# Kernel tuning notes

Hardware: AMD Instinct MI355X
Metric: run time of the kernel (lower is better)

## Reference

```python
import jax, jax.numpy as jnp
import numpy as np

B, C, T = 8, 256, 8192
K, DIL = 2, 2            # kernel_size, dilation (layer_i=1)
CAUSE = (K - 1) * DIL    # shift_diff when pad_input == 0


def _dconv(x, w, b):
    # dilated causal-style Conv1d, VALID padding: (B,C,T) -> (B,C,T-CAUSE)
    y = jax.lax.conv_general_dilated(
        x, w, window_strides=(1,), padding='VALID',
        rhs_dilation=(DIL,), dimension_numbers=('NCH', 'OIH', 'NCH'))
    return y + b[None, :, None]


def setup_inputs() -> dict:
    key = jax.random.key(0)
    ks = jax.random.split(key, 20)
    f = lambda k, s: jax.random.normal(k, s, dtype=jnp.float32)
    w = lambda k, s: f(k, s) * 0.05
    return {
        'x': f(ks[0], (B, C, T)),
        'cin': f(ks[1], (B, C, T)),
        'gin': f(ks[2], (B, C, T)),
        'skips': f(ks[3], (B, C, T)),
        # filter (tanh) branch convs
        'w_fx': w(ks[4], (C, C, K)), 'b_fx': w(ks[5], (C,)),
        'w_fc': w(ks[6], (C, C, K)), 'b_fc': w(ks[7], (C,)),
        'w_fg': w(ks[8], (C, C, K)), 'b_fg': w(ks[9], (C,)),
        # gate (sigmoid) branch convs
        'w_gx': w(ks[10], (C, C, K)), 'b_gx': w(ks[11], (C,)),
        'w_gc': w(ks[12], (C, C, K)), 'b_gc': w(ks[13], (C,)),
        'w_gg': w(ks[14], (C, C, K)), 'b_gg': w(ks[15], (C,)),
        # 1x1 residual and skip convs
        'w_res': w(ks[16], (C, C)), 'b_res': w(ks[17], (C,)),
        'w_skip': w(ks[18], (C, C)), 'b_skip': w(ks[19], (C,)),
    }


def reference(x, cin, gin, skips,
              w_fx, b_fx, w_fc, b_fc, w_fg, b_fg,
              w_gx, b_gx, w_gc, b_gc, w_gg, b_gg,
              w_res, b_res, w_skip, b_skip):
    # GatedUnit(AddPaths(conv_x, conv_cin, conv_gin)):
    f = jnp.tanh(_dconv(x, w_fx, b_fx) + _dconv(cin, w_fc, b_fc) + _dconv(gin, w_fg, b_fg))
    g = jax.nn.sigmoid(_dconv(x, w_gx, b_gx) + _dconv(cin, w_gc, b_gc) + _dconv(gin, w_gg, b_gg))
    y = f * g                                   # (B, C, T-CAUSE)
    # Skips: 1x1 conv + accumulate with (sliced) incoming skips
    skips_out = jnp.einsum('oc,bct->bot', w_skip, y) + b_skip[None, :, None] + skips[:, :, CAUSE:]
    # residual 1x1 conv + accum with sliced input (accum_outputs=-1)
    res = jnp.einsum('oc,bct->bot', w_res, y) + b_res[None, :, None] + x[:, :, CAUSE:]
    return (res, cin[:, :, CAUSE:], gin[:, :, CAUSE:], skips_out)
```

## Files before the change

### kernel.cpp

```cpp
#include <hip/hip_runtime.h>
#include <stdint.h>

#define B_   8
#define C_   256
#define T_   8192
#define TOUT 8190

typedef float  f32x4  __attribute__((ext_vector_type(4)));
typedef float  f32x2  __attribute__((ext_vector_type(2)));
typedef __bf16 bf16x8 __attribute__((ext_vector_type(8)));

#define W1_OFF 0
#define W2_OFF 1572864
#define B1_OFF 1835008
#define B2_OFF 1837056
#define N_W1 (512 * 1536)
#define N_W2 (512 * 256)

static __device__ __forceinline__ unsigned short f2bf(float x) {
  union { float f; uint32_t u; } v; v.f = x;
  uint32_t r = v.u + 0x7fffu + ((v.u >> 16) & 1u);
  return (unsigned short)(r >> 16);
}

__global__ __launch_bounds__(256) void prep_kernel(
    const float* w_fx, const float* w_fc, const float* w_fg,
    const float* w_gx, const float* w_gc, const float* w_gg,
    const float* b_fx, const float* b_fc, const float* b_fg,
    const float* b_gx, const float* b_gc, const float* b_gg,
    const float* w_res, const float* b_res,
    const float* w_skip, const float* b_skip,
    char* ws) {
  int idx = blockIdx.x * 256 + threadIdx.x;
  unsigned short* w1p = (unsigned short*)(ws + W1_OFF);
  unsigned short* w2p = (unsigned short*)(ws + W2_OFF);
  float* bias1 = (float*)(ws + B1_OFF);
  float* bias2 = (float*)(ws + B2_OFF);
  if (idx < N_W1) {
    int m = idx / 1536, k = idx - m * 1536;
    int src = k >> 9, rem = k & 511, ci = rem >> 1, tap = rem & 1;
    int cout = m >> 1, br = m & 1;
    const float* wp = (br == 0) ? (src == 0 ? w_fx : (src == 1 ? w_fc : w_fg))
                                : (src == 0 ? w_gx : (src == 1 ? w_gc : w_gg));
    float val = wp[cout * 512 + ci * 2 + tap];
    int mf = m >> 4, ml = m & 15, kf = k >> 5, kl = k & 31, kq = kl >> 3, j = kl & 7;
    w1p[(size_t)(kf * 32 + mf) * 512 + (kq * 16 + ml) * 8 + j] = f2bf(val);
  } else if (idx < N_W1 + N_W2) {
    int i2 = idx - N_W1;
    int m = i2 >> 8, k = i2 & 255;
    float val = (m < 256) ? w_res[m * 256 + k] : w_skip[(m - 256) * 256 + k];
    int mf = m >> 4, ml = m & 15, kf = k >> 5, kl = k & 31, kq = kl >> 3, j = kl & 7;
    w2p[(size_t)(kf * 32 + mf) * 512 + (kq * 16 + ml) * 8 + j] = f2bf(val);
  } else if (idx < N_W1 + N_W2 + 1024) {
    int i3 = idx - N_W1 - N_W2;
    if (i3 < 512) {
      int c = i3 >> 1;
      bias1[i3] = (i3 & 1) ? (b_gx[c] + b_gc[c] + b_gg[c])
                           : (b_fx[c] + b_fc[c] + b_fg[c]);
    } else {
      int m = i3 - 512;
      bias2[m] = (m < 256) ? b_res[m] : b_skip[m - 256];
    }
  }
}

__global__ __launch_bounds__(512, 4) void wavenet_kernel(
    const float* __restrict__ x, const float* __restrict__ cin,
    const float* __restrict__ gin, const float* __restrict__ skips,
    const char* __restrict__ ws, float* __restrict__ out) {
  __shared__ __align__(16) char smem[34816];
  short* Z0 = (short*)smem;
  short* Z1 = Z0 + 64 * 136;
  char*  Yb = smem;

  const unsigned short* w1p = (const unsigned short*)(ws + W1_OFF);
  const unsigned short* w2p = (const unsigned short*)(ws + W2_OFF);
  const float* bias1 = (const float*)(ws + B1_OFF);
  const float* bias2 = (const float*)(ws + B2_OFF);

  const int tid = threadIdx.x;
  const int w = tid >> 6, lane = tid & 63, ln = lane & 15, kq = lane >> 4;
  const int bb = blockIdx.x >> 7, tile = blockIdx.x & 127;
  const int t0 = tile * 64;
  const int valid = min(64, TOUT - t0);
  const int tb = t0 + w * 8;

  float* out0 = out;
  float* out1 = out + (size_t)B_ * C_ * TOUT;
  float* out2 = out + 2 * (size_t)B_ * C_ * TOUT;
  float* out3 = out + 3 * (size_t)B_ * C_ * TOUT;

  f32x4 acc[4][4];
#pragma unroll
  for (int i = 0; i < 4; ++i)
#pragma unroll
    for (int j = 0; j < 4; ++j) acc[i][j] = (f32x4){0.f, 0.f, 0.f, 0.f};

  auto issue = [&](int ch, f32x4& A, f32x4& Bv, f32x4& Cv) {
    const int s = ch >> 2, c0 = (ch & 3) * 64;
    const float* src = (s == 0) ? x : (s == 1) ? cin : gin;
    const float* p = src + ((size_t)(bb * C_ + c0 + lane)) * T_;
    A  = *(const f32x4*)(p + min(tb,     T_ - 4));
    Bv = *(const f32x4*)(p + min(tb + 4, T_ - 4));
    Cv = *(const f32x4*)(p + min(tb + 8, T_ - 4));
  };
  auto writeZ = [&](int ch, short* Zb, const f32x4& A, const f32x4& Bv,
                    const f32x4& Cv) {
    float F[10] = {A.x, A.y, A.z, A.w, Bv.x, Bv.y, Bv.z, Bv.w, Cv.x, Cv.y};
    unsigned short bv[10];
#pragma unroll
    for (int j = 0; j < 10; ++j) bv[j] = f2bf(F[j]);
#pragma unroll
    for (int j = 0; j < 8; ++j) {
      uint32_t pk = (uint32_t)bv[j] | ((uint32_t)bv[j + 2] << 16);
      *(uint32_t*)&Zb[(w * 8 + j) * 136 + lane * 2] = pk;
    }
    const int s = ch >> 2, c0 = (ch & 3) * 64;
    if (s) {
      float* o = (s == 1 ? out1 : out2) + ((size_t)(bb * C_ + c0 + lane)) * TOUT + tb;
#pragma unroll
      for (int j = 0; j < 4; ++j) {
        if (tb + 2 * j + 1 < TOUT) {
          f32x2 v = {F[2 + 2 * j], F[3 + 2 * j]};
          *(f32x2*)(o + 2 * j) = v;
        }
      }
    }
  };
  auto mfmaZ = [&](int ch, const short* Zb) {
    const int base = ch * 4;
#pragma unroll
    for (int kf = 0; kf < 4; ++kf) {
      bf16x8 zfr[4];
#pragma unroll
      for (int ni = 0; ni < 4; ++ni)
        zfr[ni] = *(const bf16x8*)&Zb[(ni * 16 + ln) * 136 + kf * 32 + kq * 8];
#pragma unroll
      for (int mi = 0; mi < 4; ++mi) {
        const bf16x8 wf = *(const bf16x8*)
            &w1p[(size_t)((base + kf) * 32 + (w * 4 + mi)) * 512 + lane * 8];
#pragma unroll
        for (int ni = 0; ni < 4; ++ni)
          acc[mi][ni] = __builtin_amdgcn_mfma_f32_16x16x32_bf16(
              wf, zfr[ni], acc[mi][ni], 0, 0, 0);
      }
    }
  };

  {
    f32x4 A, Bv, Cv;
    issue(0, A, Bv, Cv);
    writeZ(0, Z0, A, Bv, Cv);
  }
  __syncthreads();
  for (int i = 0; i < 12; ++i) {
    f32x4 A, Bv, Cv;
    if (i < 11) issue(i + 1, A, Bv, Cv);
    mfmaZ(i, (i & 1) ? Z1 : Z0);
    if (i < 11) writeZ(i + 1, (i & 1) ? Z0 : Z1, A, Bv, Cv);
    __syncthreads();
  }

#pragma unroll
  for (int mi = 0; mi < 4; ++mi) {
    const int mbase = w * 64 + mi * 16 + kq * 4;
    const f32x4 b4 = *(const f32x4*)&bias1[mbase];
#pragma unroll
    for (int ni = 0; ni < 4; ++ni) {
      f32x4 v = acc[mi][ni];
      float f0 = v.x + b4.x, g0 = v.y + b4.y, f1 = v.z + b4.z, g1 = v.w + b4.w;
      float y0 = (2.f / (1.f + __expf(-2.f * f0)) - 1.f) * (1.f / (1.f + __expf(-g0)));
      float y1 = (2.f / (1.f + __expf(-2.f * f1)) - 1.f) * (1.f / (1.f + __expf(-g1)));
      int n = ni * 16 + ln;
      uint32_t pk = (uint32_t)f2bf(y0) | ((uint32_t)f2bf(y1) << 16);
      int boff = (n * 512 + mbase) ^ ((n & 7) << 4);
      *(uint32_t*)(Yb + boff) = pk;
    }
  }
  __syncthreads();

  f32x4 acc2[4][4];
#pragma unroll
  for (int i = 0; i < 4; ++i)
#pragma unroll
    for (int j = 0; j < 4; ++j) acc2[i][j] = (f32x4){0.f, 0.f, 0.f, 0.f};

#pragma unroll
  for (int kf = 0; kf < 8; ++kf) {
    bf16x8 zfr[4];
#pragma unroll
    for (int ni = 0; ni < 4; ++ni) {
      int n = ni * 16 + ln;
      int boff = (n * 512 + kf * 64 + kq * 16) ^ ((n & 7) << 4);
      zfr[ni] = *(const bf16x8*)(Yb + boff);
    }
#pragma unroll
    for (int mi = 0; mi < 4; ++mi) {
      const bf16x8 wf = *(const bf16x8*)
          &w2p[(size_t)(kf * 32 + (w * 4 + mi)) * 512 + lane * 8];
#pragma unroll
      for (int ni = 0; ni < 4; ++ni)
        acc2[mi][ni] = __builtin_amdgcn_mfma_f32_16x16x32_bf16(
            wf, zfr[ni], acc2[mi][ni], 0, 0, 0);
    }
  }

#pragma unroll
  for (int mi = 0; mi < 4; ++mi) {
    const int mbase = w * 64 + mi * 16 + kq * 4;
    const f32x4 b4 = *(const f32x4*)&bias2[mbase];
#pragma unroll
    for (int r = 0; r < 4; ++r) {
      const int m2 = mbase + r;
      const int isres = (m2 < 256);
      const int crow = isres ? m2 : m2 - 256;
      const float* ap = (isres ? x : skips) + ((size_t)(bb * C_ + crow)) * T_ + t0 + 2;
      float* dp = (isres ? out0 : out3) + ((size_t)(bb * C_ + crow)) * TOUT + t0;
      const float bs = b4[r];
#pragma unroll
      for (int ni = 0; ni < 4; ++ni) {
        int n = ni * 16 + ln;
        if (n < valid) dp[n] = acc2[mi][ni][r] + bs + ap[n];
      }
    }
  }
}

extern "C" void kernel_launch(void* const* d_in, const int* in_sizes, int n_in,
                              void* d_out, int out_size, void* d_ws, size_t ws_size,
                              hipStream_t stream) {
  const float* xx    = (const float*)d_in[0];
  const float* cin   = (const float*)d_in[1];
  const float* gin   = (const float*)d_in[2];
  const float* skips = (const float*)d_in[3];
  const float* w_fx = (const float*)d_in[4],  *b_fx = (const float*)d_in[5];
  const float* w_fc = (const float*)d_in[6],  *b_fc = (const float*)d_in[7];
  const float* w_fg = (const float*)d_in[8],  *b_fg = (const float*)d_in[9];
  const float* w_gx = (const float*)d_in[10], *b_gx = (const float*)d_in[11];
  const float* w_gc = (const float*)d_in[12], *b_gc = (const float*)d_in[13];
  const float* w_gg = (const float*)d_in[14], *b_gg = (const float*)d_in[15];
  const float* w_res  = (const float*)d_in[16], *b_res  = (const float*)d_in[17];
  const float* w_skip = (const float*)d_in[18], *b_skip = (const float*)d_in[19];
  char* ws = (char*)d_ws;
  float* outp = (float*)d_out;

  prep_kernel<<<(N_W1 + N_W2 + 1024) / 256, 256, 0, stream>>>(
      w_fx, w_fc, w_fg, w_gx, w_gc, w_gg,
      b_fx, b_fc, b_fg, b_gx, b_gc, b_gg,
      w_res, b_res, w_skip, b_skip, ws);

  wavenet_kernel<<<1024, 512, 0, stream>>>(xx, cin, gin, skips, ws, outp);
}
```

Measured before the change: 338.0 us.

## Deepen global-load prefetch to two chunks and use LDS-only barriers with priority hints

The main loop now keeps two chunks of input loads in flight, unrolled by two with fixed register sets, so global latency is covered by an extra MFMA stage. __syncthreads is replaced by a barrier that waits only on LDS counters, so outstanding global loads no longer stall the barrier. Weight fragments for all four m-tiles are hoisted ahead of the MFMA block, and s_setprio raises wave priority during the MFMA sections. The cost is higher register pressure from the extra in-flight buffers, which may lower occupancy.

```diff
diff --git a/kernel.cpp b/kernel.cpp
--- a/kernel.cpp
+++ b/kernel.cpp
@@ -16,6 +16,13 @@
 #define B2_OFF 1837056
 #define N_W1 (512 * 1536)
 #define N_W2 (512 * 256)
+
+#define LBAR() do {                                          \
+    asm volatile("s_waitcnt lgkmcnt(0)" ::: "memory");       \
+    __builtin_amdgcn_sched_barrier(0);                       \
+    __builtin_amdgcn_s_barrier();                            \
+    __builtin_amdgcn_sched_barrier(0);                       \
+  } while (0)
 
 static __device__ __forceinline__ unsigned short f2bf(float x) {
   union { float f; uint32_t u; } v; v.f = x;
@@ -129,36 +136,43 @@
   };
   auto mfmaZ = [&](int ch, const short* Zb) {
     const int base = ch * 4;
+    __builtin_amdgcn_s_setprio(1);
 #pragma unroll
     for (int kf = 0; kf < 4; ++kf) {
       bf16x8 zfr[4];
 #pragma unroll
       for (int ni = 0; ni < 4; ++ni)
         zfr[ni] = *(const bf16x8*)&Zb[(ni * 16 + ln) * 136 + kf * 32 + kq * 8];
-#pragma unroll
-      for (int mi = 0; mi < 4; ++mi) {
-        const bf16x8 wf = *(const bf16x8*)
+      bf16x8 wfr[4];
+#pragma unroll
+      for (int mi = 0; mi < 4; ++mi)
+        wfr[mi] = *(const bf16x8*)
             &w1p[(size_t)((base + kf) * 32 + (w * 4 + mi)) * 512 + lane * 8];
+#pragma unroll
+      for (int mi = 0; mi < 4; ++mi)
 #pragma unroll
         for (int ni = 0; ni < 4; ++ni)
           acc[mi][ni] = __builtin_amdgcn_mfma_f32_16x16x32_bf16(
-              wf, zfr[ni], acc[mi][ni], 0, 0, 0);
-      }
-    }
+              wfr[mi], zfr[ni], acc[mi][ni], 0, 0, 0);
+    }
+    __builtin_amdgcn_s_setprio(0);
   };
 
-  {
-    f32x4 A, Bv, Cv;
-    issue(0, A, Bv, Cv);
-    writeZ(0, Z0, A, Bv, Cv);
-  }
-  __syncthreads();
-  for (int i = 0; i < 12; ++i) {
-    f32x4 A, Bv, Cv;
-    if (i < 11) issue(i + 1, A, Bv, Cv);
-    mfmaZ(i, (i & 1) ? Z1 : Z0);
-    if (i < 11) writeZ(i + 1, (i & 1) ? Z0 : Z1, A, Bv, Cv);
-    __syncthreads();
+  f32x4 A0, B0v, C0v, A1, B1v, C1v;
+  issue(0, A0, B0v, C0v);
+  issue(1, A1, B1v, C1v);
+  writeZ(0, Z0, A0, B0v, C0v);
+  LBAR();
+  for (int ii = 0; ii < 6; ++ii) {
+    const int i0 = 2 * ii;
+    if (i0 + 2 < 12) issue(i0 + 2, A0, B0v, C0v);
+    mfmaZ(i0, Z0);
+    writeZ(i0 + 1, Z1, A1, B1v, C1v);
+    LBAR();
+    if (i0 + 3 < 12) issue(i0 + 3, A1, B1v, C1v);
+    mfmaZ(i0 + 1, Z1);
+    if (i0 + 2 < 12) writeZ(i0 + 2, Z0, A0, B0v, C0v);
+    LBAR();
   }
 
 #pragma unroll
@@ -177,7 +191,7 @@
       *(uint32_t*)(Yb + boff) = pk;
     }
   }
-  __syncthreads();
+  LBAR();
 
   f32x4 acc2[4][4];
 #pragma unroll
@@ -185,6 +199,7 @@
 #pragma unroll
     for (int j = 0; j < 4; ++j) acc2[i][j] = (f32x4){0.f, 0.f, 0.f, 0.f};
 
+  __builtin_amdgcn_s_setprio(1);
 #pragma unroll
   for (int kf = 0; kf < 8; ++kf) {
     bf16x8 zfr[4];
@@ -194,16 +209,19 @@
       int boff = (n * 512 + kf * 64 + kq * 16) ^ ((n & 7) << 4);
       zfr[ni] = *(const bf16x8*)(Yb + boff);
     }
-#pragma unroll
-    for (int mi = 0; mi < 4; ++mi) {
-      const bf16x8 wf = *(const bf16x8*)
+    bf16x8 wfr[4];
+#pragma unroll
+    for (int mi = 0; mi < 4; ++mi)
+      wfr[mi] = *(const bf16x8*)
           &w2p[(size_t)(kf * 32 + (w * 4 + mi)) * 512 + lane * 8];
+#pragma unroll
+    for (int mi = 0; mi < 4; ++mi)
 #pragma unroll
       for (int ni = 0; ni < 4; ++ni)
         acc2[mi][ni] = __builtin_amdgcn_mfma_f32_16x16x32_bf16(
-            wf, zfr[ni], acc2[mi][ni], 0, 0, 0);
-    }
-  }
+            wfr[mi], zfr[ni], acc2[mi][ni], 0, 0, 0);
+  }
+  __builtin_amdgcn_s_setprio(0);
 
 #pragma unroll
   for (int mi = 0; mi < 4; ++mi) {
```

Measured after the change: 395.7 us. 17.1% more time.
